# Kernel tuning notes

Hardware: AMD Instinct MI355X
Metric: run time of the kernel (lower is better)

Reference implementation:

```python
import jax, jax.numpy as jnp
import numpy as np

B, S, D, F, E, K = 2, 2048, 1024, 4096, 8, 2

def setup_inputs() -> dict:
    key = jax.random.key(0)
    ks = jax.random.split(key, 5)
    x = jax.random.normal(ks[0], (B, S, D), dtype=jnp.float32)
    Wg = jax.random.normal(ks[1], (D, E), dtype=jnp.float32) * 0.02   # gate (fp32)
    W1 = jax.random.normal(ks[2], (E, D, F), dtype=jnp.float32) * 0.02  # expert fc1
    b1 = jnp.zeros((E, F), dtype=jnp.float32)
    W2 = jax.random.normal(ks[3], (E, F, D), dtype=jnp.float32) * 0.02  # expert fc2
    b2 = jnp.zeros((E, D), dtype=jnp.float32)
    return {"x": x, "Wg": Wg, "W1": W1, "b1": b1, "W2": W2, "b2": b2}

def reference(x, Wg, W1, b1, W2, b2):
    b, s, d = x.shape
    e = Wg.shape[1]
    T = b * s
    C = (2 * K * T) // e  # generous capacity -> effectively no token drops
    xt = x.reshape(T, d)

    # --- top-2 gating (fp32) ---
    logits = xt.astype(jnp.float32) @ Wg.astype(jnp.float32)  # [T,E]
    gates = jax.nn.softmax(logits, axis=-1)
    idx1 = jnp.argmax(gates, axis=-1)                      # [T]
    mask1 = jax.nn.one_hot(idx1, e, dtype=gates.dtype)     # [T,E]
    gate1 = jnp.sum(gates * mask1, axis=-1)                # [T]
    logits2 = jnp.where(mask1 > 0, -jnp.inf, logits)
    idx2 = jnp.argmax(logits2, axis=-1)
    mask2 = jax.nn.one_hot(idx2, e, dtype=gates.dtype)
    gate2 = jnp.sum(gates * mask2, axis=-1)
    denom = gate1 + gate2 + 1e-9
    w1 = gate1 / denom
    w2 = gate2 / denom

    # --- capacity-based slot assignment (GShard-style) ---
    p1 = jnp.cumsum(mask1, axis=0) - mask1                 # earlier same-expert tokens
    pos1 = jnp.sum(p1 * mask1, axis=-1).astype(jnp.int32)  # [T]
    off = jnp.sum(mask1, axis=0)                           # [E] 1st-choice counts
    p2 = jnp.cumsum(mask2, axis=0) - mask2 + off[None, :]
    pos2 = jnp.sum(p2 * mask2, axis=-1).astype(jnp.int32)
    keep1 = (pos1 < C).astype(xt.dtype)
    keep2 = (pos2 < C).astype(xt.dtype)
    pos1 = jnp.clip(pos1, 0, C - 1)
    pos2 = jnp.clip(pos2, 0, C - 1)

    # --- dispatch (scatter tokens to expert slots) ---
    xe = jnp.zeros((e, C, d), dtype=xt.dtype)
    xe = xe.at[idx1, pos1].add(xt * keep1[:, None])
    xe = xe.at[idx2, pos2].add(xt * keep2[:, None])

    # --- grouped expert FFN: gelu(x W1 + b1) W2 + b2 ---
    h = jax.nn.gelu(jnp.einsum('ecd,edf->ecf', xe, W1) + b1[:, None, :], approximate=False)
    ye = jnp.einsum('ecf,efd->ecd', h, W2) + b2[:, None, :]  # [E,C,D]

    # --- combine (gather + weighted sum) ---
    out = ye[idx1, pos1] * (w1 * keep1)[:, None] + ye[idx2, pos2] * (w2 * keep2)[:, None]
    return out.reshape(b, s, d)
```

## Files before the change

kernel.cpp:

```cpp
#include <hip/hip_runtime.h>
#include <hip/hip_bf16.h>
#include <math.h>

#define Dv 1024
#define Fv 4096
#define Ev 8
#define Tt 4096
#define CAP 2048
#define NROW 8192
#define RPAD 128

typedef unsigned int u32;
typedef __bf16 bf16x8 __attribute__((ext_vector_type(8)));
typedef float f32x4 __attribute__((ext_vector_type(4)));

__device__ __forceinline__ unsigned short f2bf(float f) {
  u32 u = __float_as_uint(f);
  u32 r = (u + 0x7fffu + ((u >> 16) & 1u)) >> 16;
  return (unsigned short)r;
}

__device__ __forceinline__ void gload_lds16(const void* g, void* l) {
  __builtin_amdgcn_global_load_lds(
      (const __attribute__((address_space(1))) u32*)g,
      (__attribute__((address_space(3))) u32*)l, 16, 0, 0);
}

__global__ void __launch_bounds__(256)
transpose_bf16_kernel(const float* __restrict__ src, unsigned short* __restrict__ dst,
                      int R, int Cc) {
  __shared__ float tile[64][65];
  int e = blockIdx.z;
  src += (size_t)e * R * Cc;
  dst += (size_t)e * R * Cc;
  int c0 = blockIdx.x * 64, r0 = blockIdx.y * 64;
  int tc = threadIdx.x & 63, tr = threadIdx.x >> 6;
#pragma unroll
  for (int i = tr; i < 64; i += 4)
    tile[i][tc] = src[(size_t)(r0 + i) * Cc + (c0 + tc)];
  __syncthreads();
  int rp = (threadIdx.x & 31) * 2, co = threadIdx.x >> 5;
#pragma unroll
  for (int k = 0; k < 8; ++k) {
    int c = co + 8 * k;
    ushort2 v;
    v.x = f2bf(tile[rp][c]);
    v.y = f2bf(tile[rp + 1][c]);
    *(ushort2*)&dst[(size_t)(c0 + c) * R + (r0 + rp)] = v;
  }
}

__global__ void __launch_bounds__(256)
gating_kernel(const float* __restrict__ x, const float* __restrict__ Wg,
              int* __restrict__ idx1, int* __restrict__ idx2,
              float* __restrict__ w1, float* __restrict__ w2) {
  int t = blockIdx.x * 4 + (threadIdx.x >> 6);
  int lane = threadIdx.x & 63;
  const float* xr = x + (size_t)t * Dv;
  float acc[Ev];
#pragma unroll
  for (int e = 0; e < Ev; ++e) acc[e] = 0.f;
#pragma unroll
  for (int j = 0; j < 4; ++j) {
    int dbase = (lane + 64 * j) * 4;
    float4 xv = *(const float4*)(xr + dbase);
    const float* wr = Wg + (size_t)dbase * Ev;
#pragma unroll
    for (int u = 0; u < 4; ++u) {
      float xd = (&xv.x)[u];
#pragma unroll
      for (int e = 0; e < Ev; ++e) acc[e] += xd * wr[u * Ev + e];
    }
  }
#pragma unroll
  for (int off = 32; off > 0; off >>= 1) {
#pragma unroll
    for (int e = 0; e < Ev; ++e) acc[e] += __shfl_xor(acc[e], off, 64);
  }
  if (lane == 0) {
    float mx = acc[0]; int i1 = 0;
#pragma unroll
    for (int e = 1; e < Ev; ++e) { if (acc[e] > mx) { mx = acc[e]; i1 = e; } }
    float ge[Ev]; float se = 0.f;
#pragma unroll
    for (int e = 0; e < Ev; ++e) { ge[e] = expf(acc[e] - mx); se += ge[e]; }
    float mx2 = -INFINITY; int i2 = 0; bool have = false;
#pragma unroll
    for (int e = 0; e < Ev; ++e) {
      if (e == i1) continue;
      if (!have || acc[e] > mx2) { mx2 = acc[e]; i2 = e; have = true; }
    }
    float g1 = 0.f, g2 = 0.f;
#pragma unroll
    for (int e = 0; e < Ev; ++e) { if (e == i1) g1 = ge[e]; if (e == i2) g2 = ge[e]; }
    g1 /= se; g2 /= se;
    float denom = g1 + g2 + 1e-9f;
    idx1[t] = i1; idx2[t] = i2;
    w1[t] = g1 / denom; w2[t] = g2 / denom;
  }
}

__global__ void __launch_bounds__(256)
scan_kernel(const int* __restrict__ gidx1, const int* __restrict__ gidx2,
            const float* __restrict__ gw1, const float* __restrict__ gw2,
            int* __restrict__ ci1, int* __restrict__ ci2,
            float* __restrict__ w1k, float* __restrict__ w2k,
            int* __restrict__ n_e, int* __restrict__ base_e) {
  __shared__ short s1[Tt], s2[Tt];
  __shared__ int c1[256][Ev], c2[256][Ev];
  __shared__ int tot1[Ev], tot2[Ev], sne[Ev], sbase[Ev];
  int tid = threadIdx.x;
  for (int i = tid; i < Tt; i += 256) { s1[i] = (short)gidx1[i]; s2[i] = (short)gidx2[i]; }
  __syncthreads();
  int base = tid * 16;
  {
    int l1[Ev], l2[Ev];
#pragma unroll
    for (int e = 0; e < Ev; ++e) { l1[e] = 0; l2[e] = 0; }
    for (int j = 0; j < 16; ++j) {
      int a = s1[base + j], b = s2[base + j];
#pragma unroll
      for (int e = 0; e < Ev; ++e) { l1[e] += (a == e); l2[e] += (b == e); }
    }
#pragma unroll
    for (int e = 0; e < Ev; ++e) { c1[tid][e] = l1[e]; c2[tid][e] = l2[e]; }
  }
  __syncthreads();
  if (tid < 2 * Ev) {
    int e = tid & 7;
    int* col = (tid < Ev) ? &c1[0][e] : &c2[0][e];
    int run = 0;
    for (int c = 0; c < 256; ++c) { int v = col[(size_t)c * Ev]; col[(size_t)c * Ev] = run; run += v; }
    if (tid < Ev) tot1[e] = run; else tot2[e] = run;
  }
  __syncthreads();
  if (tid == 0) {
    int b = 0;
#pragma unroll
    for (int e = 0; e < Ev; ++e) {
      int ne = tot1[e] + tot2[e];
      ne = ne < CAP ? ne : CAP;
      sne[e] = ne; sbase[e] = b;
      n_e[e] = ne; base_e[e] = b;
      b += ne;
    }
  }
  __syncthreads();
  int r1[Ev], r2[Ev];
#pragma unroll
  for (int e = 0; e < Ev; ++e) { r1[e] = c1[tid][e]; r2[e] = c2[tid][e] + tot1[e]; }
  for (int j = 0; j < 16; ++j) {
    int tk = base + j;
    int e1 = s1[tk], e2 = s2[tk];
    int p1 = 0, p2 = 0;
#pragma unroll
    for (int e = 0; e < Ev; ++e) {
      if (e == e1) { p1 = r1[e]; r1[e]++; }
      if (e == e2) { p2 = r2[e]; r2[e]++; }
    }
    bool k1 = p1 < CAP, k2 = p2 < CAP;
    ci1[tk] = k1 ? (sbase[e1] + p1) : -1;
    ci2[tk] = k2 ? (sbase[e2] + p2) : -1;
    w1k[tk] = k1 ? gw1[tk] : 0.f;
    w2k[tk] = k2 ? gw2[tk] : 0.f;
  }
}

__global__ void __launch_bounds__(256)
dispatch_kernel(const float* __restrict__ x,
                const int* __restrict__ ci1, const int* __restrict__ ci2,
                unsigned short* __restrict__ Xe) {
  int t = blockIdx.x, tid = threadIdx.x;
  float4 xv = *(const float4*)(x + (size_t)t * Dv + tid * 4);
  ushort4 bv;
  bv.x = f2bf(xv.x); bv.y = f2bf(xv.y); bv.z = f2bf(xv.z); bv.w = f2bf(xv.w);
  int c1 = ci1[t], c2 = ci2[t];
  if (c1 >= 0) *(ushort4*)(Xe + (size_t)c1 * Dv + tid * 4) = bv;
  if (c2 >= 0) *(ushort4*)(Xe + (size_t)c2 * Dv + tid * 4) = bv;
}

template <int MODE, int SPLITS>
__global__ void __launch_bounds__(256, 2)
gemm_kernel(const unsigned short* __restrict__ A,
            const unsigned short* __restrict__ Bt,
            const float* __restrict__ bias,
            void* __restrict__ Out,
            const int* __restrict__ n_e, const int* __restrict__ base_e,
            int N, int K) {
  int e = blockIdx.x;
  int zz = blockIdx.z;
  int split = zz % SPLITS, mt = zz / SPLITS;
  int m0 = mt * 128;
  int ne = n_e[e];
  if (m0 >= ne) return;
  int rbase = base_e[e];
  int n0 = blockIdx.y * 128;
  const int kchunk = K / SPLITS;
  A += ((size_t)(rbase + m0)) * K + (size_t)split * kchunk;
  Bt += (size_t)e * N * K + (size_t)n0 * K + (size_t)split * kchunk;
  bias += (size_t)e * N;

  __shared__ unsigned short As[128 * 64];
  __shared__ unsigned short Bs[128 * 64];
  int tid = threadIdx.x;
  int wave = tid >> 6, lane = tid & 63;
  int wm = (wave & 1) * 64, wn = (wave >> 1) * 64;
  int quad = lane >> 4, lr = lane & 15;
  int sw = lr & 7;
  f32x4 acc[4][4];
#pragma unroll
  for (int i = 0; i < 4; ++i)
#pragma unroll
    for (int j = 0; j < 4; ++j)
#pragma unroll
      for (int r = 0; r < 4; ++r) acc[i][j][r] = 0.f;

  int r_st = tid >> 3;
  int g_st = tid & 7;
  int gsrc = g_st ^ (r_st & 7);
  const unsigned short* gA = A + (size_t)r_st * K + gsrc * 8;
  const unsigned short* gB = Bt + (size_t)r_st * K + gsrc * 8;
  unsigned short* lA = &As[tid * 8];
  unsigned short* lB = &Bs[tid * 8];

  for (int k0 = 0; k0 < kchunk; k0 += 64) {
    __syncthreads();
#pragma unroll
    for (int s = 0; s < 4; ++s) {
      gload_lds16(gA + (size_t)(s * 32) * K + k0, lA + s * 2048);
      gload_lds16(gB + (size_t)(s * 32) * K + k0, lB + s * 2048);
    }
    __syncthreads();
#pragma unroll
    for (int h = 0; h < 2; ++h) {
      bf16x8 af[4], bfr[4];
#pragma unroll
      for (int mi = 0; mi < 4; ++mi) {
        int row = wm + mi * 16 + lr;
        int c = (h * 4 + quad) ^ sw;
        af[mi] = *(const bf16x8*)&As[row * 64 + c * 8];
      }
#pragma unroll
      for (int ni = 0; ni < 4; ++ni) {
        int row = wn + ni * 16 + lr;
        int c = (h * 4 + quad) ^ sw;
        bfr[ni] = *(const bf16x8*)&Bs[row * 64 + c * 8];
      }
#pragma unroll
      for (int mi = 0; mi < 4; ++mi)
#pragma unroll
        for (int ni = 0; ni < 4; ++ni)
          acc[mi][ni] = __builtin_amdgcn_mfma_f32_16x16x32_bf16(af[mi], bfr[ni], acc[mi][ni], 0, 0, 0);
    }
  }

#pragma unroll
  for (int ni = 0; ni < 4; ++ni) {
    int col = n0 + wn + ni * 16 + lr;
    float bv = (MODE == 0 || split == 0) ? bias[col] : 0.f;
#pragma unroll
    for (int mi = 0; mi < 4; ++mi) {
#pragma unroll
      for (int r = 0; r < 4; ++r) {
        int rowl = m0 + wm + mi * 16 + quad * 4 + r;
        if (rowl < ne) {
          size_t grow = (size_t)(rbase + rowl);
          float v = acc[mi][ni][r] + bv;
          if (MODE == 0) {
            v = 0.5f * v * (1.0f + erff(v * 0.70710678118654752f));
            ((unsigned short*)Out)[grow * N + col] = f2bf(v);
          } else {
            ((float*)Out)[((size_t)split * NROW + grow) * N + col] = v;
          }
        }
      }
    }
  }
}

__global__ void __launch_bounds__(256)
combine_kernel(const float* __restrict__ ye,
               const int* __restrict__ ci1, const int* __restrict__ ci2,
               const float* __restrict__ w1k, const float* __restrict__ w2k,
               float* __restrict__ out) {
  int t = blockIdx.x, tid = threadIdx.x;
  int c1 = ci1[t], c2 = ci2[t];
  float a1 = w1k[t], a2 = w2k[t];
  const float* ye1 = ye + (size_t)NROW * Dv;
  float4 o = make_float4(0.f, 0.f, 0.f, 0.f);
  if (c1 >= 0) {
    float4 y0 = *(const float4*)(ye + (size_t)c1 * Dv + tid * 4);
    float4 y1 = *(const float4*)(ye1 + (size_t)c1 * Dv + tid * 4);
    o.x += a1 * (y0.x + y1.x); o.y += a1 * (y0.y + y1.y);
    o.z += a1 * (y0.z + y1.z); o.w += a1 * (y0.w + y1.w);
  }
  if (c2 >= 0) {
    float4 y0 = *(const float4*)(ye + (size_t)c2 * Dv + tid * 4);
    float4 y1 = *(const float4*)(ye1 + (size_t)c2 * Dv + tid * 4);
    o.x += a2 * (y0.x + y1.x); o.y += a2 * (y0.y + y1.y);
    o.z += a2 * (y0.z + y1.z); o.w += a2 * (y0.w + y1.w);
  }
  *(float4*)(out + (size_t)t * Dv + tid * 4) = o;
}

extern "C" void kernel_launch(void* const* d_in, const int* in_sizes, int n_in,
                              void* d_out, int out_size, void* d_ws, size_t ws_size,
                              hipStream_t stream) {
  const float* x  = (const float*)d_in[0];
  const float* Wg = (const float*)d_in[1];
  const float* W1 = (const float*)d_in[2];
  const float* b1 = (const float*)d_in[3];
  const float* W2 = (const float*)d_in[4];
  const float* b2 = (const float*)d_in[5];
  float* out = (float*)d_out;

  char* p = (char*)d_ws;
  size_t off = 0;
  auto alloc = [&](size_t bytes) {
    void* q = p + off;
    off += (bytes + 255) & ~(size_t)255;
    return q;
  };
  unsigned short* Wt1 = (unsigned short*)alloc((size_t)Ev * Fv * Dv * 2);
  unsigned short* Wt2 = (unsigned short*)alloc((size_t)Ev * Dv * Fv * 2);
  unsigned short* Xe  = (unsigned short*)alloc((size_t)(NROW + RPAD) * Dv * 2);
  unsigned short* h   = (unsigned short*)alloc((size_t)(NROW + RPAD) * Fv * 2);
  int*   idx1 = (int*)alloc(Tt * 4);
  int*   idx2 = (int*)alloc(Tt * 4);
  int*   ci1  = (int*)alloc(Tt * 4);
  int*   ci2  = (int*)alloc(Tt * 4);
  float* w1   = (float*)alloc(Tt * 4);
  float* w2   = (float*)alloc(Tt * 4);
  float* w1k  = (float*)alloc(Tt * 4);
  float* w2k  = (float*)alloc(Tt * 4);
  int*   n_e  = (int*)alloc(Ev * 4);
  int*   base = (int*)alloc(Ev * 4);
  float* ye   = (float*)Wt1;

  transpose_bf16_kernel<<<dim3(Fv / 64, Dv / 64, Ev), 256, 0, stream>>>(W1, Wt1, Dv, Fv);
  gating_kernel<<<Tt / 4, 256, 0, stream>>>(x, Wg, idx1, idx2, w1, w2);
  scan_kernel<<<1, 256, 0, stream>>>(idx1, idx2, w1, w2, ci1, ci2, w1k, w2k, n_e, base);
  dispatch_kernel<<<Tt, 256, 0, stream>>>(x, ci1, ci2, Xe);
  gemm_kernel<0, 1><<<dim3(Ev, Fv / 128, CAP / 128), 256, 0, stream>>>(
      Xe, Wt1, b1, h, n_e, base, Fv, Dv);
  transpose_bf16_kernel<<<dim3(Dv / 64, Fv / 64, Ev), 256, 0, stream>>>(W2, Wt2, Fv, Dv);
  gemm_kernel<1, 2><<<dim3(Ev, Dv / 128, (CAP / 128) * 2), 256, 0, stream>>>(
      h, Wt2, b2, ye, n_e, base, Dv, Fv);
  combine_kernel<<<Tt, 256, 0, stream>>>(ye, ci1, ci2, w1k, w2k, out);
}
```

Before: 634.4 us.

## Fuse transposes with gating, drop split-K in fc2, store bf16 expert output

Merges both weight transposes and the gating computation into a single launch. Replaces the serial column scan with a wave-shuffle parallel scan. Changes the second GEMM from split-K with two fp32 partial outputs to a single pass over the full K using 128x64 tiles. The expert output is stored as bf16, so the combine kernel reads half as many bytes and no longer sums partials. This removes launches and memory traffic, but rounds the expert output to bf16 (less precision) and gives up the split-K parallelism.

Result: faster. 586.3 us (-7.6%).

```diff
diff --git a/kernel.cpp b/kernel.cpp
--- a/kernel.cpp
+++ b/kernel.cpp
@@ -20,20 +20,29 @@
   return (unsigned short)r;
 }
 
+__device__ __forceinline__ float bf2f(unsigned short s) {
+  u32 u = ((u32)s) << 16;
+  return __uint_as_float(u);
+}
+
 __device__ __forceinline__ void gload_lds16(const void* g, void* l) {
   __builtin_amdgcn_global_load_lds(
       (const __attribute__((address_space(1))) u32*)g,
       (__attribute__((address_space(3))) u32*)l, 16, 0, 0);
 }
 
-__global__ void __launch_bounds__(256)
-transpose_bf16_kernel(const float* __restrict__ src, unsigned short* __restrict__ dst,
-                      int R, int Cc) {
-  __shared__ float tile[64][65];
-  int e = blockIdx.z;
+__device__ __forceinline__ void do_transpose(const float* __restrict__ src,
+                                             unsigned short* __restrict__ dst,
+                                             int R, int Cc, int bid,
+                                             float (*tile)[65]) {
+  int ctiles = Cc >> 6;
+  int rtiles = R >> 6;
+  int cx = bid % ctiles;
+  int ry = (bid / ctiles) % rtiles;
+  int e = bid / (ctiles * rtiles);
   src += (size_t)e * R * Cc;
   dst += (size_t)e * R * Cc;
-  int c0 = blockIdx.x * 64, r0 = blockIdx.y * 64;
+  int c0 = cx * 64, r0 = ry * 64;
   int tc = threadIdx.x & 63, tr = threadIdx.x >> 6;
 #pragma unroll
   for (int i = tr; i < 64; i += 4)
@@ -51,10 +60,22 @@
 }
 
 __global__ void __launch_bounds__(256)
-gating_kernel(const float* __restrict__ x, const float* __restrict__ Wg,
-              int* __restrict__ idx1, int* __restrict__ idx2,
-              float* __restrict__ w1, float* __restrict__ w2) {
-  int t = blockIdx.x * 4 + (threadIdx.x >> 6);
+pre_kernel(const float* __restrict__ W1, unsigned short* __restrict__ Wt1,
+           const float* __restrict__ W2, unsigned short* __restrict__ Wt2,
+           const float* __restrict__ x, const float* __restrict__ Wg,
+           int* __restrict__ idx1, int* __restrict__ idx2,
+           float* __restrict__ w1, float* __restrict__ w2) {
+  __shared__ float tile[64][65];
+  int bid = blockIdx.x;
+  if (bid < 8192) {
+    do_transpose(W1, Wt1, Dv, Fv, bid, tile);
+    return;
+  }
+  if (bid < 16384) {
+    do_transpose(W2, Wt2, Fv, Dv, bid - 8192, tile);
+    return;
+  }
+  int t = (bid - 16384) * 4 + (threadIdx.x >> 6);
   int lane = threadIdx.x & 63;
   const float* xr = x + (size_t)t * Dv;
   float acc[Ev];
@@ -107,8 +128,9 @@
             float* __restrict__ w1k, float* __restrict__ w2k,
             int* __restrict__ n_e, int* __restrict__ base_e) {
   __shared__ short s1[Tt], s2[Tt];
-  __shared__ int c1[256][Ev], c2[256][Ev];
-  __shared__ int tot1[Ev], tot2[Ev], sne[Ev], sbase[Ev];
+  __shared__ int cnt[2][256][Ev];
+  __shared__ int tot[2][Ev];
+  __shared__ int sbase[Ev];
   int tid = threadIdx.x;
   for (int i = tid; i < Tt; i += 256) { s1[i] = (short)gidx1[i]; s2[i] = (short)gidx2[i]; }
   __syncthreads();
@@ -123,24 +145,43 @@
       for (int e = 0; e < Ev; ++e) { l1[e] += (a == e); l2[e] += (b == e); }
     }
 #pragma unroll
-    for (int e = 0; e < Ev; ++e) { c1[tid][e] = l1[e]; c2[tid][e] = l2[e]; }
-  }
-  __syncthreads();
-  if (tid < 2 * Ev) {
-    int e = tid & 7;
-    int* col = (tid < Ev) ? &c1[0][e] : &c2[0][e];
-    int run = 0;
-    for (int c = 0; c < 256; ++c) { int v = col[(size_t)c * Ev]; col[(size_t)c * Ev] = run; run += v; }
-    if (tid < Ev) tot1[e] = run; else tot2[e] = run;
+    for (int e = 0; e < Ev; ++e) { cnt[0][tid][e] = l1[e]; cnt[1][tid][e] = l2[e]; }
+  }
+  __syncthreads();
+  {
+    int wave = tid >> 6, lane = tid & 63;
+#pragma unroll
+    for (int q = 0; q < 4; ++q) {
+      int col = wave * 4 + q;
+      int arr = col >> 3, e = col & 7;
+      int* cp = &cnt[arr][0][e];
+      int v0 = cp[(lane * 4 + 0) * Ev];
+      int v1 = cp[(lane * 4 + 1) * Ev];
+      int v2 = cp[(lane * 4 + 2) * Ev];
+      int v3 = cp[(lane * 4 + 3) * Ev];
+      int sum = v0 + v1 + v2 + v3;
+      int incl = sum;
+#pragma unroll
+      for (int off = 1; off < 64; off <<= 1) {
+        int tval = __shfl_up(incl, off, 64);
+        if (lane >= off) incl += tval;
+      }
+      int excl = incl - sum;
+      cp[(lane * 4 + 0) * Ev] = excl;
+      cp[(lane * 4 + 1) * Ev] = excl + v0;
+      cp[(lane * 4 + 2) * Ev] = excl + v0 + v1;
+      cp[(lane * 4 + 3) * Ev] = excl + v0 + v1 + v2;
+      if (lane == 63) tot[arr][e] = incl;
+    }
   }
   __syncthreads();
   if (tid == 0) {
     int b = 0;
 #pragma unroll
     for (int e = 0; e < Ev; ++e) {
-      int ne = tot1[e] + tot2[e];
+      int ne = tot[0][e] + tot[1][e];
       ne = ne < CAP ? ne : CAP;
-      sne[e] = ne; sbase[e] = b;
+      sbase[e] = b;
       n_e[e] = ne; base_e[e] = b;
       b += ne;
     }
@@ -148,7 +189,10 @@
   __syncthreads();
   int r1[Ev], r2[Ev];
 #pragma unroll
-  for (int e = 0; e < Ev; ++e) { r1[e] = c1[tid][e]; r2[e] = c2[tid][e] + tot1[e]; }
+  for (int e = 0; e < Ev; ++e) {
+    r1[e] = cnt[0][tid][e];
+    r2[e] = cnt[1][tid][e] + tot[0][e];
+  }
   for (int j = 0; j < 16; ++j) {
     int tk = base + j;
     int e1 = s1[tk], e2 = s2[tk];
@@ -179,39 +223,37 @@
   if (c2 >= 0) *(ushort4*)(Xe + (size_t)c2 * Dv + tid * 4) = bv;
 }
 
-template <int MODE, int SPLITS>
+template <int MODE, int BN>
 __global__ void __launch_bounds__(256, 2)
 gemm_kernel(const unsigned short* __restrict__ A,
             const unsigned short* __restrict__ Bt,
             const float* __restrict__ bias,
-            void* __restrict__ Out,
+            unsigned short* __restrict__ Out,
             const int* __restrict__ n_e, const int* __restrict__ base_e,
             int N, int K) {
+  constexpr int NI = BN / 32;
   int e = blockIdx.x;
-  int zz = blockIdx.z;
-  int split = zz % SPLITS, mt = zz / SPLITS;
-  int m0 = mt * 128;
+  int m0 = blockIdx.z * 128;
   int ne = n_e[e];
   if (m0 >= ne) return;
   int rbase = base_e[e];
-  int n0 = blockIdx.y * 128;
-  const int kchunk = K / SPLITS;
-  A += ((size_t)(rbase + m0)) * K + (size_t)split * kchunk;
-  Bt += (size_t)e * N * K + (size_t)n0 * K + (size_t)split * kchunk;
+  int n0 = blockIdx.y * BN;
+  A += ((size_t)(rbase + m0)) * K;
+  Bt += (size_t)e * N * K + (size_t)n0 * K;
   bias += (size_t)e * N;
 
   __shared__ unsigned short As[128 * 64];
-  __shared__ unsigned short Bs[128 * 64];
+  __shared__ unsigned short Bs[BN * 64];
   int tid = threadIdx.x;
   int wave = tid >> 6, lane = tid & 63;
-  int wm = (wave & 1) * 64, wn = (wave >> 1) * 64;
+  int wm = (wave & 1) * 64, wn = (wave >> 1) * (BN / 2);
   int quad = lane >> 4, lr = lane & 15;
   int sw = lr & 7;
-  f32x4 acc[4][4];
+  f32x4 acc[4][NI];
 #pragma unroll
   for (int i = 0; i < 4; ++i)
 #pragma unroll
-    for (int j = 0; j < 4; ++j)
+    for (int j = 0; j < NI; ++j)
 #pragma unroll
       for (int r = 0; r < 4; ++r) acc[i][j][r] = 0.f;
 
@@ -223,17 +265,18 @@
   unsigned short* lA = &As[tid * 8];
   unsigned short* lB = &Bs[tid * 8];
 
-  for (int k0 = 0; k0 < kchunk; k0 += 64) {
+  for (int k0 = 0; k0 < K; k0 += 64) {
     __syncthreads();
 #pragma unroll
-    for (int s = 0; s < 4; ++s) {
+    for (int s = 0; s < 4; ++s)
       gload_lds16(gA + (size_t)(s * 32) * K + k0, lA + s * 2048);
+#pragma unroll
+    for (int s = 0; s < BN / 32; ++s)
       gload_lds16(gB + (size_t)(s * 32) * K + k0, lB + s * 2048);
-    }
     __syncthreads();
 #pragma unroll
     for (int h = 0; h < 2; ++h) {
-      bf16x8 af[4], bfr[4];
+      bf16x8 af[4], bfr[NI];
 #pragma unroll
       for (int mi = 0; mi < 4; ++mi) {
         int row = wm + mi * 16 + lr;
@@ -241,7 +284,7 @@
         af[mi] = *(const bf16x8*)&As[row * 64 + c * 8];
       }
 #pragma unroll
-      for (int ni = 0; ni < 4; ++ni) {
+      for (int ni = 0; ni < NI; ++ni) {
         int row = wn + ni * 16 + lr;
         int c = (h * 4 + quad) ^ sw;
         bfr[ni] = *(const bf16x8*)&Bs[row * 64 + c * 8];
@@ -249,15 +292,15 @@
 #pragma unroll
       for (int mi = 0; mi < 4; ++mi)
 #pragma unroll
-        for (int ni = 0; ni < 4; ++ni)
+        for (int ni = 0; ni < NI; ++ni)
           acc[mi][ni] = __builtin_amdgcn_mfma_f32_16x16x32_bf16(af[mi], bfr[ni], acc[mi][ni], 0, 0, 0);
     }
   }
 
 #pragma unroll
-  for (int ni = 0; ni < 4; ++ni) {
+  for (int ni = 0; ni < NI; ++ni) {
     int col = n0 + wn + ni * 16 + lr;
-    float bv = (MODE == 0 || split == 0) ? bias[col] : 0.f;
+    float bv = bias[col];
 #pragma unroll
     for (int mi = 0; mi < 4; ++mi) {
 #pragma unroll
@@ -266,12 +309,9 @@
         if (rowl < ne) {
           size_t grow = (size_t)(rbase + rowl);
           float v = acc[mi][ni][r] + bv;
-          if (MODE == 0) {
+          if (MODE == 0)
             v = 0.5f * v * (1.0f + erff(v * 0.70710678118654752f));
-            ((unsigned short*)Out)[grow * N + col] = f2bf(v);
-          } else {
-            ((float*)Out)[((size_t)split * NROW + grow) * N + col] = v;
-          }
+          Out[grow * N + col] = f2bf(v);
         }
       }
     }
@@ -279,26 +319,23 @@
 }
 
 __global__ void __launch_bounds__(256)
-combine_kernel(const float* __restrict__ ye,
+combine_kernel(const unsigned short* __restrict__ ye,
                const int* __restrict__ ci1, const int* __restrict__ ci2,
                const float* __restrict__ w1k, const float* __restrict__ w2k,
                float* __restrict__ out) {
   int t = blockIdx.x, tid = threadIdx.x;
   int c1 = ci1[t], c2 = ci2[t];
   float a1 = w1k[t], a2 = w2k[t];
-  const float* ye1 = ye + (size_t)NROW * Dv;
   float4 o = make_float4(0.f, 0.f, 0.f, 0.f);
   if (c1 >= 0) {
-    float4 y0 = *(const float4*)(ye + (size_t)c1 * Dv + tid * 4);
-    float4 y1 = *(const float4*)(ye1 + (size_t)c1 * Dv + tid * 4);
-    o.x += a1 * (y0.x + y1.x); o.y += a1 * (y0.y + y1.y);
-    o.z += a1 * (y0.z + y1.z); o.w += a1 * (y0.w + y1.w);
+    ushort4 y = *(const ushort4*)(ye + (size_t)c1 * Dv + tid * 4);
+    o.x += a1 * bf2f(y.x); o.y += a1 * bf2f(y.y);
+    o.z += a1 * bf2f(y.z); o.w += a1 * bf2f(y.w);
   }
   if (c2 >= 0) {
-    float4 y0 = *(const float4*)(ye + (size_t)c2 * Dv + tid * 4);
-    float4 y1 = *(const float4*)(ye1 + (size_t)c2 * Dv + tid * 4);
-    o.x += a2 * (y0.x + y1.x); o.y += a2 * (y0.y + y1.y);
-    o.z += a2 * (y0.z + y1.z); o.w += a2 * (y0.w + y1.w);
+    ushort4 y = *(const ushort4*)(ye + (size_t)c2 * Dv + tid * 4);
+    o.x += a2 * bf2f(y.x); o.y += a2 * bf2f(y.y);
+    o.z += a2 * bf2f(y.z); o.w += a2 * bf2f(y.w);
   }
   *(float4*)(out + (size_t)t * Dv + tid * 4) = o;
 }
@@ -335,16 +372,14 @@
   float* w2k  = (float*)alloc(Tt * 4);
   int*   n_e  = (int*)alloc(Ev * 4);
   int*   base = (int*)alloc(Ev * 4);
-  float* ye   = (float*)Wt1;
-
-  transpose_bf16_kernel<<<dim3(Fv / 64, Dv / 64, Ev), 256, 0, stream>>>(W1, Wt1, Dv, Fv);
-  gating_kernel<<<Tt / 4, 256, 0, stream>>>(x, Wg, idx1, idx2, w1, w2);
+  unsigned short* ye = Wt1;
+
+  pre_kernel<<<17408, 256, 0, stream>>>(W1, Wt1, W2, Wt2, x, Wg, idx1, idx2, w1, w2);
   scan_kernel<<<1, 256, 0, stream>>>(idx1, idx2, w1, w2, ci1, ci2, w1k, w2k, n_e, base);
   dispatch_kernel<<<Tt, 256, 0, stream>>>(x, ci1, ci2, Xe);
-  gemm_kernel<0, 1><<<dim3(Ev, Fv / 128, CAP / 128), 256, 0, stream>>>(
+  gemm_kernel<0, 128><<<dim3(Ev, Fv / 128, CAP / 128), 256, 0, stream>>>(
       Xe, Wt1, b1, h, n_e, base, Fv, Dv);
-  transpose_bf16_kernel<<<dim3(Dv / 64, Fv / 64, Ev), 256, 0, stream>>>(W2, Wt2, Fv, Dv);
-  gemm_kernel<1, 2><<<dim3(Ev, Dv / 128, (CAP / 128) * 2), 256, 0, stream>>>(
+  gemm_kernel<1, 64><<<dim3(Ev, Dv / 64, CAP / 128), 256, 0, stream>>>(
       h, Wt2, b2, ye, n_e, base, Dv, Fv);
   combine_kernel<<<Tt, 256, 0, stream>>>(ye, ci1, ci2, w1k, w2k, out);
 }
```
